# Kernel tuning notes

Hardware: AMD Instinct MI355X
Metric: run time of the kernel (lower is better)

## Reference

```python
import jax, jax.numpy as jnp
import numpy as np

B, N, K = 4, 40960, 16
D_IN, D_OUT = 32, 64


def setup_inputs() -> dict:
    key = jax.random.key(0)
    keys = iter(jax.random.split(key, 48))
    def nrm(shape, scale):
        return (jax.random.normal(next(keys), shape, jnp.float32) * scale).astype(jnp.float32)
    inp = {
        "feature": jax.random.normal(next(keys), (B, N, D_IN), jnp.float32),
        "xyz": jax.random.uniform(next(keys), (B, N, 3), jnp.float32),
        "neigh_idx": jax.random.randint(next(keys), (B, N, K), 0, N, jnp.int32),
    }
    def conv_bn(name, cin, cout):
        inp["w_" + name] = nrm((cin, cout), (2.0 / cin) ** 0.5)
        inp["s_" + name] = 1.0 + nrm((cout,), 0.1)  # folded BN scale: gamma/sqrt(var+eps)
        inp["b_" + name] = nrm((cout,), 0.1)        # folded BN bias: beta - mean*scale
    conv_bn("mlp1", D_IN, D_OUT // 2)
    conv_bn("lfa1", 10, D_OUT // 2)
    inp["w_att1_fc"] = nrm((D_OUT, D_OUT), (2.0 / D_OUT) ** 0.5)
    conv_bn("att1_mlp", D_OUT, D_OUT // 2)
    conv_bn("lfa2", D_OUT // 2, D_OUT // 2)
    inp["w_att2_fc"] = nrm((D_OUT, D_OUT), (2.0 / D_OUT) ** 0.5)
    conv_bn("att2_mlp", D_OUT, D_OUT)
    conv_bn("mlp2", D_OUT, 2 * D_OUT)
    conv_bn("sc", D_IN, 2 * D_OUT)
    return inp


def _gather(pc, idx):
    # pc: [B,N,D], idx: [B,N,K] -> [B,N,K,D]
    b, n, k = idx.shape
    flat = jnp.take_along_axis(pc, idx.reshape(b, n * k, 1), axis=1)
    return flat.reshape(b, n, k, pc.shape[-1])


def _cb(x, w, s, b, relu=True):
    # 1x1 conv + folded BN (+ ReLU), channels-last
    y = jnp.einsum('...i,io->...o', x, w) * s + b
    return jnp.maximum(y, 0.0) if relu else y


def _att_pool(fs, w_fc, w, s, b):
    # fs: [B,N,K,C]; softmax-attention pooling over K, then mlp
    scores = jax.nn.softmax(jnp.einsum('bnkc,cd->bnkd', fs, w_fc), axis=2)
    agg = jnp.sum(fs * scores, axis=2)  # [B,N,C]
    return _cb(agg, w, s, b)


def _rel_pos(xyz, idx):
    nbr = _gather(xyz, idx)                           # [B,N,K,3]
    tile = jnp.broadcast_to(xyz[:, :, None, :], nbr.shape)
    rel = tile - nbr
    dist = jnp.sqrt(jnp.sum(rel * rel, axis=-1, keepdims=True))
    return jnp.concatenate([dist, rel, tile, nbr], axis=-1)  # [B,N,K,10]


def reference(feature, xyz, neigh_idx,
              w_mlp1, s_mlp1, b_mlp1,
              w_lfa1, s_lfa1, b_lfa1,
              w_att1_fc, w_att1_mlp, s_att1_mlp, b_att1_mlp,
              w_lfa2, s_lfa2, b_lfa2,
              w_att2_fc, w_att2_mlp, s_att2_mlp, b_att2_mlp,
              w_mlp2, s_mlp2, b_mlp2,
              w_sc, s_sc, b_sc):
    f_pc = _cb(feature, w_mlp1, s_mlp1, b_mlp1)                   # [B,N,d/2]
    f_xyz = _cb(_rel_pos(xyz, neigh_idx), w_lfa1, s_lfa1, b_lfa1)  # [B,N,K,d/2]
    f_nb = _gather(f_pc, neigh_idx)                                # [B,N,K,d/2]
    f_agg = _att_pool(jnp.concatenate([f_nb, f_xyz], axis=-1),
                      w_att1_fc, w_att1_mlp, s_att1_mlp, b_att1_mlp)  # [B,N,d/2]
    f_xyz2 = _cb(f_xyz, w_lfa2, s_lfa2, b_lfa2)                    # [B,N,K,d/2]
    f_nb2 = _gather(f_agg, neigh_idx)                              # [B,N,K,d/2]
    f_pc2 = _att_pool(jnp.concatenate([f_nb2, f_xyz2], axis=-1),
                      w_att2_fc, w_att2_mlp, s_att2_mlp, b_att2_mlp)  # [B,N,d]
    out = _cb(f_pc2, w_mlp2, s_mlp2, b_mlp2, relu=False)           # [B,N,2d]
    sc = _cb(feature, w_sc, s_sc, b_sc, relu=False)
    return jax.nn.leaky_relu(out + sc, negative_slope=0.2)
```

## Files before the change

### kernel.cpp

```cpp
#include <hip/hip_runtime.h>
#include <hip/hip_bf16.h>

#define NPTS  40960
#define BNPTS 163840
#define KNB   16

#define PK_MLP1 0
#define PK_FC1  1280
#define PK_FC2  6912
#define PK_L1   12544
#define PK_L2   13824
#define PK_M1   15104
#define PK_M2   17920
#define PK_W2   23552
#define PK_WS   34816
#define PK_TOTAL 39936

using bf16x8 = __attribute__((ext_vector_type(8))) short;
using f32x4  = __attribute__((ext_vector_type(4))) float;

__device__ __forceinline__ unsigned short f2bf(float x) {
    union { float f; unsigned u; } v; v.f = x;
    unsigned r = v.u + 0x7fffu + ((v.u >> 16) & 1u);
    return (unsigned short)(r >> 16);
}
__device__ __forceinline__ float bf2f(unsigned short u) {
    union { unsigned u; float f; } v; v.u = ((unsigned)u) << 16;
    return v.f;
}
__device__ __forceinline__ unsigned pk2(float lo, float hi) {
    union { __hip_bfloat162 h; unsigned u; } v;
    v.h = __float22bfloat162_rn(float2{lo, hi});
    return v.u;
}
__device__ __forceinline__ bf16x8 pack8(float a0, float a1, float a2, float a3,
                                        float a4, float a5, float a6, float a7) {
    union { unsigned u[4]; bf16x8 v; } w;
    w.u[0] = pk2(a0, a1); w.u[1] = pk2(a2, a3);
    w.u[2] = pk2(a4, a5); w.u[3] = pk2(a6, a7);
    return w.v;
}
__device__ __forceinline__ f32x4 mfma16(bf16x8 a, bf16x8 b, f32x4 c) {
    return __builtin_amdgcn_mfma_f32_16x16x32_bf16(a, b, c, 0, 0, 0);
}
__device__ __forceinline__ float exp2_fast(float x) { return __builtin_amdgcn_exp2f(x); }
__device__ __forceinline__ float rcp_fast(float x)  { return __builtin_amdgcn_rcpf(x); }

__global__ __launch_bounds__(256)
void k_prep(const float* __restrict__ wm1, const float* __restrict__ wfc1,
            const float* __restrict__ wfc2,
            const float* __restrict__ wlfa1, const float* __restrict__ slfa1, const float* __restrict__ blfa1,
            const float* __restrict__ wlfa2,
            const float* __restrict__ wam1, const float* __restrict__ wam2,
            const float* __restrict__ w2, const float* __restrict__ wsc,
            unsigned short* __restrict__ pk)
{
    const int tid = threadIdx.x, blk = blockIdx.x;
    const float LOG2E = 1.4426950408889634f;
    switch (blk) {
    case 0:
        for (int t = tid; t < 32 * 32; t += 256) {
            int c = t >> 5, d = t & 31;
            int slot = (d & 1) * 16 + (d >> 1);
            pk[PK_MLP1 + slot * 40 + c] = f2bf(wm1[t]);
        }
        break;
    case 1:
        for (int t = tid; t < 64 * 64; t += 256) {
            int c = t >> 6, d = t & 63;
            pk[PK_FC1 + d * 88 + c] = f2bf(wfc1[t] * LOG2E);
        }
        break;
    case 2:
        for (int t = tid; t < 64 * 64; t += 256) {
            int c = t >> 6, d = t & 63;
            pk[PK_FC2 + d * 88 + c] = f2bf(wfc2[t] * LOG2E);
        }
        break;
    case 3:
        for (int t = tid; t < 32 * 32; t += 256) {
            int k = t >> 5, d = t & 31;
            int slot = (d & 1) * 16 + (d >> 1);
            float v1 = k < 10 ? wlfa1[k * 32 + d] * slfa1[d] : (k == 10 ? blfa1[d] : 0.f);
            pk[PK_L1 + slot * 40 + k] = f2bf(v1);
            pk[PK_L2 + slot * 40 + k] = f2bf(wlfa2[k * 32 + d]);
        }
        break;
    case 4:
        for (int t = tid; t < 64 * 32; t += 256) {
            int c = t / 32, d = t % 32;
            int slot = (d & 1) * 16 + (d >> 1);
            pk[PK_M1 + slot * 88 + c] = f2bf(wam1[t]);
        }
        break;
    case 5:
        for (int t = tid; t < 64 * 64; t += 256) {
            int c = t >> 6, d = t & 63;
            int slot = (d >> 5) * 32 + (d & 1) * 16 + ((d & 31) >> 1);
            pk[PK_M2 + slot * 88 + c] = f2bf(wam2[t]);
        }
        break;
    case 6:
        for (int t = tid; t < 64 * 128; t += 256) {
            int c = t >> 7, d = t & 127;
            int slot = (d >> 5) * 32 + (d & 1) * 16 + ((d & 31) >> 1);
            pk[PK_W2 + slot * 88 + c] = f2bf(w2[t]);
        }
        break;
    case 7:
        for (int t = tid; t < 32 * 128; t += 256) {
            int c = t >> 7, d = t & 127;
            int slot = (d >> 5) * 32 + (d & 1) * 16 + ((d & 31) >> 1);
            pk[PK_WS + slot * 40 + c] = f2bf(wsc[t]);
        }
        break;
    }
}

__global__ __launch_bounds__(256)
void k_mlp1(const float* __restrict__ feature, const unsigned short* __restrict__ pk,
            const float* __restrict__ s, const float* __restrict__ b,
            const float* __restrict__ xyz, float* __restrict__ xyz4,
            unsigned short* __restrict__ f_pc)
{
    const int tid = threadIdx.x;
    {
        int idx = blockIdx.x * 256 + tid;
        float3 v = *(const float3*)&xyz[(size_t)idx * 3];
        *(float4*)&xyz4[(size_t)idx * 4] = make_float4(v.x, v.y, v.z, 0.f);
    }
    const int lid = tid & 63, wv = tid >> 6;
    const int col = lid & 15, quad = lid >> 4;
    bf16x8 B0 = *(const bf16x8*)&pk[PK_MLP1 + col * 40 + quad * 8];
    bf16x8 B1 = *(const bf16x8*)&pk[PK_MLP1 + (16 + col) * 40 + quad * 8];
    float s0 = s[2 * col], b0 = b[2 * col], s1 = s[2 * col + 1], b1 = b[2 * col + 1];
    for (int itp = 0; itp < 4; itp++) {
        const int p0 = blockIdx.x * 256 + wv * 64 + itp * 16;
        const float* fr = &feature[(size_t)(p0 + col) * 32 + quad * 8];
        float4 u0 = *(const float4*)fr;
        float4 u1 = *(const float4*)(fr + 4);
        bf16x8 a = pack8(u0.x, u0.y, u0.z, u0.w, u1.x, u1.y, u1.z, u1.w);
        f32x4 z = {0.f, 0.f, 0.f, 0.f};
        f32x4 d0 = mfma16(a, B0, z);
        f32x4 d1 = mfma16(a, B1, z);
        #pragma unroll
        for (int r = 0; r < 4; r++) {
            int p = p0 + quad * 4 + r;
            float ye = fmaxf(d0[r] * s0 + b0, 0.f);
            float yo = fmaxf(d1[r] * s1 + b1, 0.f);
            *(unsigned*)&f_pc[(size_t)p * 32 + 2 * col] = pk2(ye, yo);
        }
    }
}

template<int NOUT, bool HAS_LFA2>
__global__ __launch_bounds__(256, 4)
void k_att(const float* __restrict__ xyz4, const int* __restrict__ nidx,
           const unsigned short* __restrict__ src,
           const unsigned short* __restrict__ wl1T, const unsigned short* __restrict__ wl2T,
           const float* __restrict__ slfa2, const float* __restrict__ blfa2,
           const unsigned short* __restrict__ wfcT, const unsigned short* __restrict__ wmT,
           const float* __restrict__ smlp, const float* __restrict__ bmlp,
           unsigned short* __restrict__ out,
           const float* __restrict__ feature,
           const unsigned short* __restrict__ w2T, const unsigned short* __restrict__ wsT,
           const float* __restrict__ s2, const float* __restrict__ b2,
           const float* __restrict__ ssc, const float* __restrict__ bsc,
           float* __restrict__ outF)
{
    constexpr int NP = NOUT / 32;
    constexpr int WS = 88;
    __shared__ __align__(16) char smem[23552];
    __shared__ __align__(16) unsigned short fp2_s[NOUT == 64 ? 4 * 1152 : 8];
    char* uni = smem;

    const int tid = threadIdx.x;
    const int lid = tid & 63, wv = tid >> 6;
    const int col = lid & 15, quad = lid >> 4;

    bf16x8 Bfc[4][2];
    #pragma unroll
    for (int nt = 0; nt < 4; nt++)
        #pragma unroll
        for (int ks = 0; ks < 2; ks++)
            Bfc[nt][ks] = *(const bf16x8*)&wfcT[(nt * 16 + col) * WS + ks * 32 + quad * 8];
    bf16x8 Bl1e = *(const bf16x8*)&wl1T[col * 40 + quad * 8];
    bf16x8 Bl1o = *(const bf16x8*)&wl1T[(16 + col) * 40 + quad * 8];
    bf16x8 Bl2e{}, Bl2o{};
    float sl2e = 0.f, bl2e = 0.f, sl2o = 0.f, bl2o = 0.f;
    if (HAS_LFA2) {
        Bl2e = *(const bf16x8*)&wl2T[col * 40 + quad * 8];
        Bl2o = *(const bf16x8*)&wl2T[(16 + col) * 40 + quad * 8];
        sl2e = slfa2[2 * col]; bl2e = blfa2[2 * col];
        sl2o = slfa2[2 * col + 1]; bl2o = blfa2[2 * col + 1];
    }
    float sme[NP], bme[NP], smo[NP], bmo[NP];
    #pragma unroll
    for (int tp = 0; tp < NP; tp++) {
        sme[tp] = smlp[tp * 32 + 2 * col]; bme[tp] = bmlp[tp * 32 + 2 * col];
        smo[tp] = smlp[tp * 32 + 2 * col + 1]; bmo[tp] = bmlp[tp * 32 + 2 * col + 1];
    }

    unsigned short* fc  = (unsigned short*)(uni) + wv * 1408;
    unsigned short* ag  = (unsigned short*)(uni + 11264) + wv * 1152;
    unsigned short* nb  = (unsigned short*)(uni + 20480) + wv * 256;
    float*          cxy = (float*)(uni + 22528) + wv * 64;
    unsigned short* fp2 = fp2_s + wv * 1152;

    const int blk = (int)blockIdx.x;
    const int vblk = (blk & 7) * 320 + (blk >> 3);
    const int pbase = vblk * 64 + wv * 16;
    const int pb = (pbase / NPTS) * NPTS;
    const unsigned short* srcb = src + (size_t)pb * 32;
    const float4* x4  = (const float4*)xyz4;
    const float4* x4b = x4 + pb;

    {
        int4 t4 = *(const int4*)&nidx[(size_t)pbase * KNB + lid * 4];
        ushort4 u = make_ushort4((unsigned short)t4.x, (unsigned short)t4.y,
                                 (unsigned short)t4.z, (unsigned short)t4.w);
        *(ushort4*)&nb[lid * 4] = u;
        if (lid < 16) *(float4*)&cxy[lid * 4] = x4[pbase + lid];
    }

    const f32x4 z = {0.f, 0.f, 0.f, 0.f};
    bf16x8 vs; float nx = 0.f, ny = 0.f, nz = 0.f;
    {
        int j = (int)nb[col];
        vs = *(const bf16x8*)(srcb + (size_t)j * 32 + quad * 8);
        if (quad < 2) { float4 t = x4b[j]; nx = t.x; ny = t.y; nz = t.z; }
    }

    #pragma unroll 1
    for (int it = 0; it < 16; it++) {
        bf16x8 a0 = vs;
        *(bf16x8*)&fc[col * WS + quad * 8] = a0;

        float cx = cxy[it * 4], cy = cxy[it * 4 + 1], cz = cxy[it * 4 + 2];
        float rx = cx - nx, ry = cy - ny, rz = cz - nz;
        float dd = sqrtf(rx * rx + ry * ry + rz * rz);
        float f0 = 0.f, f1 = 0.f, f2 = 0.f, f3 = 0.f, f4 = 0.f, f5 = 0.f, f6 = 0.f, f7 = 0.f;
        if (quad == 0)      { f0 = dd; f1 = rx; f2 = ry; f3 = rz; f4 = cx; f5 = cy; f6 = cz; f7 = nx; }
        else if (quad == 1) { f0 = ny; f1 = nz; f2 = 1.0f; }
        bf16x8 al = pack8(f0, f1, f2, f3, f4, f5, f6, f7);

        {
            int itn = it < 15 ? it + 1 : 15;
            int j = (int)nb[itn * 16 + col];
            vs = *(const bf16x8*)(srcb + (size_t)j * 32 + quad * 8);
            if (quad < 2) { float4 t = x4b[j]; nx = t.x; ny = t.y; nz = t.z; }
        }

        {
            f32x4 d0 = mfma16(al, Bl1e, z);
            f32x4 d1 = mfma16(al, Bl1o, z);
            #pragma unroll
            for (int r = 0; r < 4; r++) {
                float ye = fmaxf(d0[r], 0.f);
                float yo = fmaxf(d1[r], 0.f);
                *(unsigned*)&fc[(quad * 4 + r) * WS + 32 + 2 * col] = pk2(ye, yo);
            }
            if (HAS_LFA2) {
                bf16x8 a2 = *(const bf16x8*)&fc[col * WS + 32 + quad * 8];
                f32x4 e0 = mfma16(a2, Bl2e, z);
                f32x4 e1 = mfma16(a2, Bl2o, z);
                #pragma unroll
                for (int r = 0; r < 4; r++) {
                    float ye = fmaxf(e0[r] * sl2e + bl2e, 0.f);
                    float yo = fmaxf(e1[r] * sl2o + bl2o, 0.f);
                    *(unsigned*)&fc[(quad * 4 + r) * WS + 32 + 2 * col] = pk2(ye, yo);
                }
            }
        }

        {
            bf16x8 a1 = *(const bf16x8*)&fc[col * WS + 32 + quad * 8];
            #pragma unroll
            for (int nt = 0; nt < 4; nt++) {
                f32x4 L = mfma16(a1, Bfc[nt][1], mfma16(a0, Bfc[nt][0], z));
                float e0 = exp2_fast(L[0]), e1 = exp2_fast(L[1]);
                float e2 = exp2_fast(L[2]), e3 = exp2_fast(L[3]);
                float sden = (e0 + e1) + (e2 + e3);
                const unsigned short* frr = &fc[quad * 4 * WS + nt * 16 + col];
                float av = e0 * bf2f(frr[0]) + e1 * bf2f(frr[WS]) + e2 * bf2f(frr[2 * WS]) + e3 * bf2f(frr[3 * WS]);
                av   += __shfl_xor(av, 16, 64);
                sden += __shfl_xor(sden, 16, 64);
                av   += __shfl_xor(av, 32, 64);
                sden += __shfl_xor(sden, 32, 64);
                if (quad == 0) ag[it * 72 + nt * 16 + col] = f2bf(av * rcp_fast(sden));
            }
        }
    }

    {
        bf16x8 am0 = *(const bf16x8*)&ag[col * 72 + quad * 8];
        bf16x8 am1 = *(const bf16x8*)&ag[col * 72 + 32 + quad * 8];
        #pragma unroll
        for (int tp = 0; tp < NP; tp++) {
            bf16x8 Be0, Be1, Bo0, Bo1;
            if constexpr (NOUT == 32) {
                Be0 = *(const bf16x8*)&wmT[col * WS + quad * 8];
                Be1 = *(const bf16x8*)&wmT[col * WS + 32 + quad * 8];
                Bo0 = *(const bf16x8*)&wmT[(16 + col) * WS + quad * 8];
                Bo1 = *(const bf16x8*)&wmT[(16 + col) * WS + 32 + quad * 8];
            } else {
                Be0 = *(const bf16x8*)&wmT[(tp * 32 + col) * WS + quad * 8];
                Be1 = *(const bf16x8*)&wmT[(tp * 32 + col) * WS + 32 + quad * 8];
                Bo0 = *(const bf16x8*)&wmT[(tp * 32 + 16 + col) * WS + quad * 8];
                Bo1 = *(const bf16x8*)&wmT[(tp * 32 + 16 + col) * WS + 32 + quad * 8];
            }
            f32x4 de = mfma16(am1, Be1, mfma16(am0, Be0, z));
            f32x4 dq = mfma16(am1, Bo1, mfma16(am0, Bo0, z));
            #pragma unroll
            for (int r = 0; r < 4; r++) {
                float ye = fmaxf(de[r] * sme[tp] + bme[tp], 0.f);
                float yo = fmaxf(dq[r] * smo[tp] + bmo[tp], 0.f);
                if constexpr (NOUT == 64) {
                    *(unsigned*)&fp2[(quad * 4 + r) * 72 + tp * 32 + 2 * col] = pk2(ye, yo);
                } else {
                    int pp = pbase + quad * 4 + r;
                    *(unsigned*)&out[(size_t)pp * NOUT + tp * 32 + 2 * col] = pk2(ye, yo);
                }
            }
        }
    }

    if constexpr (NOUT == 64) {
        bf16x8 a10 = *(const bf16x8*)&fp2[col * 72 + quad * 8];
        bf16x8 a11 = *(const bf16x8*)&fp2[col * 72 + 32 + quad * 8];
        const float* fr = &feature[(size_t)(pbase + col) * 32 + quad * 8];
        float4 u0 = *(const float4*)fr;
        float4 u1 = *(const float4*)(fr + 4);
        bf16x8 a2 = pack8(u0.x, u0.y, u0.z, u0.w, u1.x, u1.y, u1.z, u1.w);
        #pragma unroll
        for (int m = 0; m < 4; m++) {
            bf16x8 ke0 = *(const bf16x8*)&w2T[(m * 32 + col) * 88 + quad * 8];
            bf16x8 ke1 = *(const bf16x8*)&w2T[(m * 32 + col) * 88 + 32 + quad * 8];
            bf16x8 ko0 = *(const bf16x8*)&w2T[(m * 32 + 16 + col) * 88 + quad * 8];
            bf16x8 ko1 = *(const bf16x8*)&w2T[(m * 32 + 16 + col) * 88 + 32 + quad * 8];
            bf16x8 se  = *(const bf16x8*)&wsT[(m * 32 + col) * 40 + quad * 8];
            bf16x8 so  = *(const bf16x8*)&wsT[(m * 32 + 16 + col) * 40 + quad * 8];
            f32x4 de = mfma16(a11, ke1, mfma16(a10, ke0, z));
            f32x4 dq = mfma16(a11, ko1, mfma16(a10, ko0, z));
            f32x4 ee = mfma16(a2, se, z);
            f32x4 eo = mfma16(a2, so, z);
            int ce = m * 32 + 2 * col, co = ce + 1;
            float sse = s2[ce], sso = s2[co];
            float ste = ssc[ce], sto = ssc[co];
            float bbe = b2[ce] + bsc[ce], bbo = b2[co] + bsc[co];
            #pragma unroll
            for (int r = 0; r < 4; r++) {
                float ye = de[r] * sse + ee[r] * ste + bbe;
                float yo = dq[r] * sso + eo[r] * sto + bbo;
                ye = ye > 0.f ? ye : 0.2f * ye;
                yo = yo > 0.f ? yo : 0.2f * yo;
                *(float2*)&outF[(size_t)(pbase + quad * 4 + r) * 128 + m * 32 + 2 * col] =
                    make_float2(ye, yo);
            }
        }
    }
}

extern "C" void kernel_launch(void* const* d_in, const int* in_sizes, int n_in,
                              void* d_out, int out_size, void* d_ws, size_t ws_size,
                              hipStream_t stream) {
    const float* feature = (const float*)d_in[0];
    const float* xyz     = (const float*)d_in[1];
    const int*   nidx    = (const int*)d_in[2];
    const float* w_mlp1 = (const float*)d_in[3];
    const float* s_mlp1 = (const float*)d_in[4];
    const float* b_mlp1 = (const float*)d_in[5];
    const float* w_lfa1 = (const float*)d_in[6];
    const float* s_lfa1 = (const float*)d_in[7];
    const float* b_lfa1 = (const float*)d_in[8];
    const float* w_att1_fc  = (const float*)d_in[9];
    const float* w_att1_mlp = (const float*)d_in[10];
    const float* s_att1_mlp = (const float*)d_in[11];
    const float* b_att1_mlp = (const float*)d_in[12];
    const float* w_lfa2 = (const float*)d_in[13];
    const float* s_lfa2 = (const float*)d_in[14];
    const float* b_lfa2 = (const float*)d_in[15];
    const float* w_att2_fc  = (const float*)d_in[16];
    const float* w_att2_mlp = (const float*)d_in[17];
    const float* s_att2_mlp = (const float*)d_in[18];
    const float* b_att2_mlp = (const float*)d_in[19];
    const float* w_mlp2 = (const float*)d_in[20];
    const float* s_mlp2 = (const float*)d_in[21];
    const float* b_mlp2 = (const float*)d_in[22];
    const float* w_sc = (const float*)d_in[23];
    const float* s_sc = (const float*)d_in[24];
    const float* b_sc = (const float*)d_in[25];

    unsigned short* f_pc  = (unsigned short*)d_ws;
    unsigned short* f_agg = f_pc  + (size_t)BNPTS * 32;
    unsigned short* f_pc2 = f_agg + (size_t)BNPTS * 32;
    unsigned short* pkw   = f_pc2 + (size_t)BNPTS * 64;
    float*          xyz4  = (float*)(pkw + PK_TOTAL);
    float* out = (float*)d_out;

    k_prep<<<8, 256, 0, stream>>>(
        w_mlp1, w_att1_fc, w_att2_fc,
        w_lfa1, s_lfa1, b_lfa1, w_lfa2,
        w_att1_mlp, w_att2_mlp, w_mlp2, w_sc, pkw);
    k_mlp1<<<BNPTS / 256, 256, 0, stream>>>(feature, pkw, s_mlp1, b_mlp1, xyz, xyz4, f_pc);
    k_att<32, false><<<BNPTS / 64, 256, 0, stream>>>(
        xyz4, nidx, f_pc,
        pkw + PK_L1, pkw + PK_L1,
        s_lfa1, b_lfa1,
        pkw + PK_FC1, pkw + PK_M1, s_att1_mlp, b_att1_mlp, f_agg,
        feature, pkw + PK_W2, pkw + PK_WS,
        s_mlp2, b_mlp2, s_sc, b_sc, out);
    k_att<64, true><<<BNPTS / 64, 256, 0, stream>>>(
        xyz4, nidx, f_agg,
        pkw + PK_L1, pkw + PK_L2,
        s_lfa2, b_lfa2,
        pkw + PK_FC2, pkw + PK_M2, s_att2_mlp, b_att2_mlp, f_pc2,
        feature, pkw + PK_W2, pkw + PK_WS,
        s_mlp2, b_mlp2, s_sc, b_sc, out);
}
```

Measured before the change: 337.3 us.

## Fuse weight prep into mlp1 kernel and run attention with single-wave blocks

The separate weight-packing kernel is folded into the mlp1 kernel: the first few blocks pack the weights, and every block builds its own bf16 copy of the mlp1 weight in shared memory. This removes one launch and the dependency on the packed mlp1 weights. The attention kernels now run one 64-thread wave per block with shared memory sized for a single wave, giving finer scheduling granularity and possibly higher occupancy. The f_pc2 buffer is dropped and f_agg is passed as the output pointer of the second pass, which appears to be an unused or aliasing output, and the kernel launches four times as many blocks.

```diff
diff --git a/kernel.cpp b/kernel.cpp
--- a/kernel.cpp
+++ b/kernel.cpp
@@ -5,7 +5,6 @@
 #define BNPTS 163840
 #define KNB   16
 
-#define PK_MLP1 0
 #define PK_FC1  1280
 #define PK_FC2  6912
 #define PK_L1   12544
@@ -47,37 +46,40 @@
 __device__ __forceinline__ float rcp_fast(float x)  { return __builtin_amdgcn_rcpf(x); }
 
 __global__ __launch_bounds__(256)
-void k_prep(const float* __restrict__ wm1, const float* __restrict__ wfc1,
-            const float* __restrict__ wfc2,
+void k_mlp1(const float* __restrict__ feature,
+            const float* __restrict__ wm1, const float* __restrict__ s, const float* __restrict__ b,
+            const float* __restrict__ wfc1, const float* __restrict__ wfc2,
             const float* __restrict__ wlfa1, const float* __restrict__ slfa1, const float* __restrict__ blfa1,
             const float* __restrict__ wlfa2,
             const float* __restrict__ wam1, const float* __restrict__ wam2,
             const float* __restrict__ w2, const float* __restrict__ wsc,
-            unsigned short* __restrict__ pk)
+            const float* __restrict__ xyz, float* __restrict__ xyz4,
+            unsigned short* __restrict__ pk,
+            unsigned short* __restrict__ f_pc)
 {
+    __shared__ unsigned short wT[32 * 40];
     const int tid = threadIdx.x, blk = blockIdx.x;
     const float LOG2E = 1.4426950408889634f;
+
+    {
+        int idx = blk * 256 + tid;
+        float3 v = *(const float3*)&xyz[(size_t)idx * 3];
+        *(float4*)&xyz4[(size_t)idx * 4] = make_float4(v.x, v.y, v.z, 0.f);
+    }
     switch (blk) {
     case 0:
-        for (int t = tid; t < 32 * 32; t += 256) {
-            int c = t >> 5, d = t & 31;
-            int slot = (d & 1) * 16 + (d >> 1);
-            pk[PK_MLP1 + slot * 40 + c] = f2bf(wm1[t]);
+        for (int t = tid; t < 64 * 64; t += 256) {
+            int c = t >> 6, d = t & 63;
+            pk[PK_FC1 + d * 88 + c] = f2bf(wfc1[t] * LOG2E);
         }
         break;
     case 1:
         for (int t = tid; t < 64 * 64; t += 256) {
             int c = t >> 6, d = t & 63;
-            pk[PK_FC1 + d * 88 + c] = f2bf(wfc1[t] * LOG2E);
+            pk[PK_FC2 + d * 88 + c] = f2bf(wfc2[t] * LOG2E);
         }
         break;
     case 2:
-        for (int t = tid; t < 64 * 64; t += 256) {
-            int c = t >> 6, d = t & 63;
-            pk[PK_FC2 + d * 88 + c] = f2bf(wfc2[t] * LOG2E);
-        }
-        break;
-    case 3:
         for (int t = tid; t < 32 * 32; t += 256) {
             int k = t >> 5, d = t & 31;
             int slot = (d & 1) * 16 + (d >> 1);
@@ -86,28 +88,28 @@
             pk[PK_L2 + slot * 40 + k] = f2bf(wlfa2[k * 32 + d]);
         }
         break;
-    case 4:
+    case 3:
         for (int t = tid; t < 64 * 32; t += 256) {
             int c = t / 32, d = t % 32;
             int slot = (d & 1) * 16 + (d >> 1);
             pk[PK_M1 + slot * 88 + c] = f2bf(wam1[t]);
         }
         break;
-    case 5:
+    case 4:
         for (int t = tid; t < 64 * 64; t += 256) {
             int c = t >> 6, d = t & 63;
             int slot = (d >> 5) * 32 + (d & 1) * 16 + ((d & 31) >> 1);
             pk[PK_M2 + slot * 88 + c] = f2bf(wam2[t]);
         }
         break;
-    case 6:
+    case 5:
         for (int t = tid; t < 64 * 128; t += 256) {
             int c = t >> 7, d = t & 127;
             int slot = (d >> 5) * 32 + (d & 1) * 16 + ((d & 31) >> 1);
             pk[PK_W2 + slot * 88 + c] = f2bf(w2[t]);
         }
         break;
-    case 7:
+    case 6:
         for (int t = tid; t < 32 * 128; t += 256) {
             int c = t >> 7, d = t & 127;
             int slot = (d >> 5) * 32 + (d & 1) * 16 + ((d & 31) >> 1);
@@ -115,27 +117,21 @@
         }
         break;
     }
-}
-
-__global__ __launch_bounds__(256)
-void k_mlp1(const float* __restrict__ feature, const unsigned short* __restrict__ pk,
-            const float* __restrict__ s, const float* __restrict__ b,
-            const float* __restrict__ xyz, float* __restrict__ xyz4,
-            unsigned short* __restrict__ f_pc)
-{
-    const int tid = threadIdx.x;
-    {
-        int idx = blockIdx.x * 256 + tid;
-        float3 v = *(const float3*)&xyz[(size_t)idx * 3];
-        *(float4*)&xyz4[(size_t)idx * 4] = make_float4(v.x, v.y, v.z, 0.f);
-    }
+
+    for (int t = tid; t < 32 * 32; t += 256) {
+        int c = t >> 5, d = t & 31;
+        int slot = (d & 1) * 16 + (d >> 1);
+        wT[slot * 40 + c] = f2bf(wm1[t]);
+    }
+    __syncthreads();
+
     const int lid = tid & 63, wv = tid >> 6;
     const int col = lid & 15, quad = lid >> 4;
-    bf16x8 B0 = *(const bf16x8*)&pk[PK_MLP1 + col * 40 + quad * 8];
-    bf16x8 B1 = *(const bf16x8*)&pk[PK_MLP1 + (16 + col) * 40 + quad * 8];
+    bf16x8 B0 = *(const bf16x8*)&wT[col * 40 + quad * 8];
+    bf16x8 B1 = *(const bf16x8*)&wT[(16 + col) * 40 + quad * 8];
     float s0 = s[2 * col], b0 = b[2 * col], s1 = s[2 * col + 1], b1 = b[2 * col + 1];
     for (int itp = 0; itp < 4; itp++) {
-        const int p0 = blockIdx.x * 256 + wv * 64 + itp * 16;
+        const int p0 = blk * 256 + wv * 64 + itp * 16;
         const float* fr = &feature[(size_t)(p0 + col) * 32 + quad * 8];
         float4 u0 = *(const float4*)fr;
         float4 u1 = *(const float4*)(fr + 4);
@@ -154,7 +150,7 @@
 }
 
 template<int NOUT, bool HAS_LFA2>
-__global__ __launch_bounds__(256, 4)
+__global__ __launch_bounds__(64, 6)
 void k_att(const float* __restrict__ xyz4, const int* __restrict__ nidx,
            const unsigned short* __restrict__ src,
            const unsigned short* __restrict__ wl1T, const unsigned short* __restrict__ wl2T,
@@ -170,12 +166,11 @@
 {
     constexpr int NP = NOUT / 32;
     constexpr int WS = 88;
-    __shared__ __align__(16) char smem[23552];
-    __shared__ __align__(16) unsigned short fp2_s[NOUT == 64 ? 4 * 1152 : 8];
+    __shared__ __align__(16) char smem[5888];
+    __shared__ __align__(16) unsigned short fp2[NOUT == 64 ? 1152 : 8];
     char* uni = smem;
 
-    const int tid = threadIdx.x;
-    const int lid = tid & 63, wv = tid >> 6;
+    const int lid = threadIdx.x;
     const int col = lid & 15, quad = lid >> 4;
 
     bf16x8 Bfc[4][2];
@@ -201,15 +196,14 @@
         smo[tp] = smlp[tp * 32 + 2 * col + 1]; bmo[tp] = bmlp[tp * 32 + 2 * col + 1];
     }
 
-    unsigned short* fc  = (unsigned short*)(uni) + wv * 1408;
-    unsigned short* ag  = (unsigned short*)(uni + 11264) + wv * 1152;
-    unsigned short* nb  = (unsigned short*)(uni + 20480) + wv * 256;
-    float*          cxy = (float*)(uni + 22528) + wv * 64;
-    unsigned short* fp2 = fp2_s + wv * 1152;
+    unsigned short* fc  = (unsigned short*)(uni);
+    unsigned short* ag  = (unsigned short*)(uni + 2816);
+    unsigned short* nb  = (unsigned short*)(uni + 5120);
+    float*          cxy = (float*)(uni + 5632);
 
     const int blk = (int)blockIdx.x;
-    const int vblk = (blk & 7) * 320 + (blk >> 3);
-    const int pbase = vblk * 64 + wv * 16;
+    const int vblk = (blk & 7) * 1280 + (blk >> 3);
+    const int pbase = vblk * 16;
     const int pb = (pbase / NPTS) * NPTS;
     const unsigned short* srcb = src + (size_t)pb * 32;
     const float4* x4  = (const float4*)xyz4;
@@ -393,28 +387,29 @@
 
     unsigned short* f_pc  = (unsigned short*)d_ws;
     unsigned short* f_agg = f_pc  + (size_t)BNPTS * 32;
-    unsigned short* f_pc2 = f_agg + (size_t)BNPTS * 32;
-    unsigned short* pkw   = f_pc2 + (size_t)BNPTS * 64;
+    unsigned short* pkw   = f_agg + (size_t)BNPTS * 32;
     float*          xyz4  = (float*)(pkw + PK_TOTAL);
     float* out = (float*)d_out;
 
-    k_prep<<<8, 256, 0, stream>>>(
-        w_mlp1, w_att1_fc, w_att2_fc,
+    k_mlp1<<<BNPTS / 256, 256, 0, stream>>>(
+        feature,
+        w_mlp1, s_mlp1, b_mlp1,
+        w_att1_fc, w_att2_fc,
         w_lfa1, s_lfa1, b_lfa1, w_lfa2,
-        w_att1_mlp, w_att2_mlp, w_mlp2, w_sc, pkw);
-    k_mlp1<<<BNPTS / 256, 256, 0, stream>>>(feature, pkw, s_mlp1, b_mlp1, xyz, xyz4, f_pc);
-    k_att<32, false><<<BNPTS / 64, 256, 0, stream>>>(
+        w_att1_mlp, w_att2_mlp, w_mlp2, w_sc,
+        xyz, xyz4, pkw, f_pc);
+    k_att<32, false><<<BNPTS / 16, 64, 0, stream>>>(
         xyz4, nidx, f_pc,
         pkw + PK_L1, pkw + PK_L1,
         s_lfa1, b_lfa1,
         pkw + PK_FC1, pkw + PK_M1, s_att1_mlp, b_att1_mlp, f_agg,
         feature, pkw + PK_W2, pkw + PK_WS,
         s_mlp2, b_mlp2, s_sc, b_sc, out);
-    k_att<64, true><<<BNPTS / 64, 256, 0, stream>>>(
+    k_att<64, true><<<BNPTS / 16, 64, 0, stream>>>(
         xyz4, nidx, f_agg,
         pkw + PK_L1, pkw + PK_L2,
         s_lfa2, b_lfa2,
-        pkw + PK_FC2, pkw + PK_M2, s_att2_mlp, b_att2_mlp, f_pc2,
+        pkw + PK_FC2, pkw + PK_M2, s_att2_mlp, b_att2_mlp, f_agg,
         feature, pkw + PK_W2, pkw + PK_WS,
         s_mlp2, b_mlp2, s_sc, b_sc, out);
 }
```

After: 354.1 us. +5.0%, slower.
